# Kernel optimization log

Hardware: AMD Instinct MI355X
Metric: run time of the kernel (lower is better)

## Reference

```python
import jax, jax.numpy as jnp
import numpy as np

B, N, D = 4, 4096, 128
LOSS_WEIGHT = 1.0  # module hardcodes self.loss_weight = 1.0


def setup_inputs() -> dict:
    key = jax.random.key(0)
    k1, k2 = jax.random.split(key)
    corr_pred = jax.random.normal(k1, (B, N, D), dtype=jnp.float32)
    corr_target = jax.random.normal(k2, (B, N, D), dtype=jnp.float32)
    return {"corr_pred": corr_pred, "corr_target": corr_target}


def chamfer_distance(x, y):
    # x: [B, N, D], y: [B, N, D]
    x2 = jnp.sum(x * x, axis=-1)                      # [B, N]  diag of x @ x^T
    y2 = jnp.sum(y * y, axis=-1)                      # [B, N]  diag of y @ y^T
    zz = jnp.einsum('bnd,bmd->bnm', x, y)             # [B, N, N]
    # P[b,i,j] = ||x_i||^2 + ||y_j||^2 - 2 x_i . y_j
    P = x2[:, :, None] + y2[:, None, :] - 2.0 * zz
    P = jnp.clip(P, 0.0, 100.0)
    return jnp.mean(jnp.min(P, axis=1)) + jnp.mean(jnp.min(P, axis=2))


def reference(corr_pred, corr_target):
    chamfer = chamfer_distance(corr_pred, corr_target)
    return LOSS_WEIGHT * chamfer / corr_target.shape[0]
```

## Files before the change

kernel.cpp:

```cpp
#include <hip/hip_runtime.h>
#include <hip/hip_bf16.h>

#define B_ 4
#define N_ 4096
#define D_ 128
#define EPB (N_ * D_)
#define COFF 1024.0f

typedef float f32x4 __attribute__((ext_vector_type(4)));
typedef int   int8v __attribute__((ext_vector_type(8)));
typedef int   int4v __attribute__((ext_vector_type(4)));

#define SQRT2 1.41421356237309515f


__global__ __launch_bounds__(256) void prep_kernel(
    const float* __restrict__ X, const float* __restrict__ Y,
    unsigned char* __restrict__ Xb, unsigned char* __restrict__ Yb,
    float* __restrict__ x2, float* __restrict__ y2,
    int* __restrict__ rowmin, int* __restrict__ colmin)
{
    const int which = blockIdx.y;
    const float* __restrict__ src = which ? Y : X;
    unsigned char* __restrict__ dst = which ? Yb : Xb;
    float* __restrict__ nrm = which ? y2 : x2;
    int* __restrict__ mn = which ? colmin : rowmin;

    const int t = threadIdx.x;
    const int r = t >> 4, c = t & 15;
    const int rgG = blockIdx.x;
    const int row = rgG * 16 + r;

    const float4 v0 = *(const float4*)(src + (size_t)row * D_ + c * 8);
    const float4 v1 = *(const float4*)(src + (size_t)row * D_ + c * 8 + 4);

    float sq = v0.x * v0.x;
    sq = fmaf(v0.y, v0.y, sq); sq = fmaf(v0.z, v0.z, sq); sq = fmaf(v0.w, v0.w, sq);
    sq = fmaf(v1.x, v1.x, sq); sq = fmaf(v1.y, v1.y, sq);
    sq = fmaf(v1.z, v1.z, sq); sq = fmaf(v1.w, v1.w, sq);
    #pragma unroll
    for (int m = 1; m < 16; m <<= 1) sq += __shfl_xor(sq, m);

    unsigned lo = 0, hi = 0;
    lo = __builtin_amdgcn_cvt_pk_fp8_f32(v0.x * SQRT2, v0.y * SQRT2, lo, false);
    lo = __builtin_amdgcn_cvt_pk_fp8_f32(v0.z * SQRT2, v0.w * SQRT2, lo, true);
    hi = __builtin_amdgcn_cvt_pk_fp8_f32(v1.x * SQRT2, v1.y * SQRT2, hi, false);
    hi = __builtin_amdgcn_cvt_pk_fp8_f32(v1.z * SQRT2, v1.w * SQRT2, hi, true);

    const int b = row >> 12;
    const int rg = (row & (N_ - 1)) >> 4;
    uint2 packed; packed.x = lo; packed.y = hi;
    *(uint2*)(dst + (size_t)b * EPB + rg * 2048 + (c >> 2) * 512
              + r * 32 + (c & 3) * 8) = packed;

    if (c == 0) {
        nrm[row] = sq;
        mn[row] = 0x7f7fffff;
    }
}

__global__ __launch_bounds__(256, 2) void chamfer_mfma(
    const unsigned char* __restrict__ Xb, const unsigned char* __restrict__ Yb,
    const float* __restrict__ x2, const float* __restrict__ y2,
    int* __restrict__ rowmin, int* __restrict__ colmin)
{
    const int b = blockIdx.z;
    const int iT = blockIdx.y;
    const int jc = blockIdx.x;
    const int tid = threadIdx.x;
    const int wave = tid >> 6, lane = tid & 63;
    const int quad = lane >> 4, l16 = lane & 15;
    const int rowBase = iT * 256 + wave * 64;

    const unsigned char* __restrict__ Xp = Xb + (size_t)b * EPB;
    const unsigned char* __restrict__ Yp = Yb + (size_t)b * EPB;

    int8v af[4];
    #pragma unroll
    for (int rt = 0; rt < 4; rt++) {
        const unsigned char* ap = Xp + ((rowBase >> 4) + rt) * 2048
                                 + quad * 512 + l16 * 32;
        const int4v lo = *(const int4v*)(ap);
        const int4v hi = *(const int4v*)(ap + 16);
        af[rt] = (int8v){lo.x, lo.y, lo.z, lo.w, hi.x, hi.y, hi.z, hi.w};
    }
    float x2v[4][4];
    #pragma unroll
    for (int rt = 0; rt < 4; rt++)
        #pragma unroll
        for (int i = 0; i < 4; i++)
            x2v[rt][i] = x2[(size_t)b * N_ + rowBase + rt * 16 + quad * 4 + i];

    float rmin[4][4];
    #pragma unroll
    for (int rt = 0; rt < 4; rt++)
        #pragma unroll
        for (int i = 0; i < 4; i++) rmin[rt][i] = 3.0e38f;

    for (int s = 0; s < 4; ++s) {
        const int colBase = jc * 256 + s * 64;
        const int cg = colBase >> 4;

        float y2v[4];
        #pragma unroll
        for (int ct = 0; ct < 4; ct++)
            y2v[ct] = y2[(size_t)b * N_ + colBase + ct * 16 + l16];

        int8v bfv[4];
        #pragma unroll
        for (int ct = 0; ct < 4; ct++) {
            const unsigned char* bp = Yp + (size_t)(cg + ct) * 2048
                                     + quad * 512 + l16 * 32;
            const int4v lo = *(const int4v*)(bp);
            const int4v hi = *(const int4v*)(bp + 16);
            bfv[ct] = (int8v){lo.x, lo.y, lo.z, lo.w, hi.x, hi.y, hi.z, hi.w};
        }

        f32x4 acc[4][4];
        #pragma unroll
        for (int i = 0; i < 4; i++)
            #pragma unroll
            for (int j = 0; j < 4; j++)
                acc[i][j] = (f32x4){0.f, 0.f, 0.f, 0.f};

        #pragma unroll
        for (int rt = 0; rt < 4; rt++)
            #pragma unroll
            for (int ct = 0; ct < 4; ct++)
                acc[rt][ct] = __builtin_amdgcn_mfma_scale_f32_16x16x128_f8f6f4(
                    af[rt], bfv[ct], acc[rt][ct],
                    0, 0,
                    0, 127,
                    0, 127);

        float cmin[4];
        #pragma unroll
        for (int ct = 0; ct < 4; ct++) cmin[ct] = 3.0e38f;
        #pragma unroll
        for (int rt = 0; rt < 4; rt++)
            #pragma unroll
            for (int i = 0; i < 4; i++) {
                const float xv = x2v[rt][i];
                float rm = rmin[rt][i];
                #pragma unroll
                for (int ct = 0; ct < 4; ct++) {
                    const float a = acc[rt][ct][i];
                    rm = fminf(rm, y2v[ct] - a);
                    cmin[ct] = fminf(cmin[ct], xv - a);
                }
                rmin[rt][i] = rm;
            }
        #pragma unroll
        for (int ct = 0; ct < 4; ct++) {
            float v = cmin[ct];
            v = fminf(v, __shfl_xor(v, 16));
            v = fminf(v, __shfl_xor(v, 32));
            if (quad == 0)
                atomicMin(&colmin[(size_t)b * N_ + colBase + ct * 16 + l16],
                          __float_as_int(v + COFF));
        }
    }

    #pragma unroll
    for (int rt = 0; rt < 4; rt++)
        #pragma unroll
        for (int i = 0; i < 4; i++) {
            float v = rmin[rt][i];
            #pragma unroll
            for (int m = 1; m < 16; m <<= 1) v = fminf(v, __shfl_xor(v, m));
            if (l16 == 0) {
                float c = fminf(fmaxf(x2v[rt][i] + v, 0.0f), 100.0f);
                atomicMin(&rowmin[(size_t)b * N_ + rowBase + rt * 16 + quad * 4 + i],
                          __float_as_int(c));
            }
        }
}

__global__ __launch_bounds__(1024) void finalize_kernel(
    const int* __restrict__ rowmin, const int* __restrict__ colmin,
    const float* __restrict__ y2, float* __restrict__ out)
{
    float s = 0.f;
    for (int i = threadIdx.x; i < B_ * N_ / 4; i += 1024) {
        int4 v = ((const int4*)rowmin)[i];
        s += __int_as_float(v.x) + __int_as_float(v.y) +
             __int_as_float(v.z) + __int_as_float(v.w);
        int4 c = ((const int4*)colmin)[i];
        float4 yv = ((const float4*)y2)[i];
        s += fminf(fmaxf(__int_as_float(c.x) - COFF + yv.x, 0.f), 100.f);
        s += fminf(fmaxf(__int_as_float(c.y) - COFF + yv.y, 0.f), 100.f);
        s += fminf(fmaxf(__int_as_float(c.z) - COFF + yv.z, 0.f), 100.f);
        s += fminf(fmaxf(__int_as_float(c.w) - COFF + yv.w, 0.f), 100.f);
    }
    #pragma unroll
    for (int m = 1; m < 64; m <<= 1) s += __shfl_xor(s, m);
    __shared__ float sm[16];
    if ((threadIdx.x & 63) == 0) sm[threadIdx.x >> 6] = s;
    __syncthreads();
    if (threadIdx.x == 0) {
        float t = 0.f;
        #pragma unroll
        for (int i = 0; i < 16; i++) t += sm[i];
        out[0] = t / ((float)B_ * (float)N_) / (float)B_;
    }
}

extern "C" void kernel_launch(void* const* d_in, const int* in_sizes, int n_in,
                              void* d_out, int out_size, void* d_ws, size_t ws_size,
                              hipStream_t stream) {
    const float* X = (const float*)d_in[0];
    const float* Y = (const float*)d_in[1];

    char* ws = (char*)d_ws;
    const size_t f8_bytes = (size_t)B_ * N_ * D_;
    unsigned char* Xb = (unsigned char*)ws;
    unsigned char* Yb = (unsigned char*)(ws + f8_bytes);
    char* ws2 = ws + 2 * f8_bytes;
    const size_t vec_bytes = (size_t)B_ * N_ * 4;
    float* x2     = (float*)(ws2);
    float* y2     = (float*)(ws2 + vec_bytes);
    int*   rowmin = (int*)  (ws2 + 2 * vec_bytes);
    int*   colmin = (int*)  (ws2 + 3 * vec_bytes);
    float* out = (float*)d_out;

    prep_kernel<<<dim3(B_ * N_ / 16, 2), 256, 0, stream>>>(
        X, Y, Xb, Yb, x2, y2, rowmin, colmin);
    chamfer_mfma<<<dim3(16, N_ / 256, B_), 256, 0, stream>>>(
        Xb, Yb, x2, y2, rowmin, colmin);
    finalize_kernel<<<1, 1024, 0, stream>>>(rowmin, colmin, y2, out);
}
```

Before: 92.60 us.

## Prefetch next Y fragment during MFMA and fold y2 into accumulator init

The loads of the next column step's fp8 Y fragments and y2 norms are issued after the current step's MFMAs and before the min-reduction epilogue, with a sched_barrier, so global-load latency overlaps compute. The MFMA accumulators now start at -y2 instead of zero, so the column min already includes the y2 term. This removes one subtract per element in the epilogue and lets finalize skip reading y2. The x2 norms are also loaded as one vector per row tile. The cost is more live registers for the double-buffered fragments, which could pressure occupancy at two blocks per CU.

```diff
diff --git a/kernel.cpp b/kernel.cpp
--- a/kernel.cpp
+++ b/kernel.cpp
@@ -84,12 +84,10 @@
         const int4v hi = *(const int4v*)(ap + 16);
         af[rt] = (int8v){lo.x, lo.y, lo.z, lo.w, hi.x, hi.y, hi.z, hi.w};
     }
-    float x2v[4][4];
+    f32x4 x2v[4];
     #pragma unroll
     for (int rt = 0; rt < 4; rt++)
-        #pragma unroll
-        for (int i = 0; i < 4; i++)
-            x2v[rt][i] = x2[(size_t)b * N_ + rowBase + rt * 16 + quad * 4 + i];
+        x2v[rt] = *(const f32x4*)(x2 + (size_t)b * N_ + rowBase + rt * 16 + quad * 4);
 
     float rmin[4][4];
     #pragma unroll
@@ -97,16 +95,10 @@
         #pragma unroll
         for (int i = 0; i < 4; i++) rmin[rt][i] = 3.0e38f;
 
-    for (int s = 0; s < 4; ++s) {
-        const int colBase = jc * 256 + s * 64;
-        const int cg = colBase >> 4;
-
-        float y2v[4];
-        #pragma unroll
-        for (int ct = 0; ct < 4; ct++)
-            y2v[ct] = y2[(size_t)b * N_ + colBase + ct * 16 + l16];
-
-        int8v bfv[4];
+    int8v bfv[4];
+    float y2v[4];
+    {
+        const int cg = (jc * 256) >> 4;
         #pragma unroll
         for (int ct = 0; ct < 4; ct++) {
             const unsigned char* bp = Yp + (size_t)(cg + ct) * 2048
@@ -114,14 +106,21 @@
             const int4v lo = *(const int4v*)(bp);
             const int4v hi = *(const int4v*)(bp + 16);
             bfv[ct] = (int8v){lo.x, lo.y, lo.z, lo.w, hi.x, hi.y, hi.z, hi.w};
-        }
+            y2v[ct] = y2[(size_t)b * N_ + jc * 256 + ct * 16 + l16];
+        }
+    }
+
+    for (int s = 0; s < 4; ++s) {
+        const int colBase = jc * 256 + s * 64;
 
         f32x4 acc[4][4];
         #pragma unroll
-        for (int i = 0; i < 4; i++)
-            #pragma unroll
-            for (int j = 0; j < 4; j++)
-                acc[i][j] = (f32x4){0.f, 0.f, 0.f, 0.f};
+        for (int ct = 0; ct < 4; ct++) {
+            const float ny = -y2v[ct];
+            #pragma unroll
+            for (int rt = 0; rt < 4; rt++)
+                acc[rt][ct] = (f32x4){ny, ny, ny, ny};
+        }
 
         #pragma unroll
         for (int rt = 0; rt < 4; rt++)
@@ -133,6 +132,20 @@
                     0, 127,
                     0, 127);
 
+        if (s < 3) {
+            const int cg = (colBase + 64) >> 4;
+            #pragma unroll
+            for (int ct = 0; ct < 4; ct++) {
+                const unsigned char* bp = Yp + (size_t)(cg + ct) * 2048
+                                         + quad * 512 + l16 * 32;
+                const int4v lo = *(const int4v*)(bp);
+                const int4v hi = *(const int4v*)(bp + 16);
+                bfv[ct] = (int8v){lo.x, lo.y, lo.z, lo.w, hi.x, hi.y, hi.z, hi.w};
+                y2v[ct] = y2[(size_t)b * N_ + colBase + 64 + ct * 16 + l16];
+            }
+        }
+        __builtin_amdgcn_sched_barrier(0);
+
         float cmin[4];
         #pragma unroll
         for (int ct = 0; ct < 4; ct++) cmin[ct] = 3.0e38f;
@@ -145,7 +158,7 @@
                 #pragma unroll
                 for (int ct = 0; ct < 4; ct++) {
                     const float a = acc[rt][ct][i];
-                    rm = fminf(rm, y2v[ct] - a);
+                    rm = fminf(rm, -a);
                     cmin[ct] = fminf(cmin[ct], xv - a);
                 }
                 rmin[rt][i] = rm;
@@ -178,7 +191,7 @@
 
 __global__ __launch_bounds__(1024) void finalize_kernel(
     const int* __restrict__ rowmin, const int* __restrict__ colmin,
-    const float* __restrict__ y2, float* __restrict__ out)
+    float* __restrict__ out)
 {
     float s = 0.f;
     for (int i = threadIdx.x; i < B_ * N_ / 4; i += 1024) {
@@ -186,11 +199,10 @@
         s += __int_as_float(v.x) + __int_as_float(v.y) +
              __int_as_float(v.z) + __int_as_float(v.w);
         int4 c = ((const int4*)colmin)[i];
-        float4 yv = ((const float4*)y2)[i];
-        s += fminf(fmaxf(__int_as_float(c.x) - COFF + yv.x, 0.f), 100.f);
-        s += fminf(fmaxf(__int_as_float(c.y) - COFF + yv.y, 0.f), 100.f);
-        s += fminf(fmaxf(__int_as_float(c.z) - COFF + yv.z, 0.f), 100.f);
-        s += fminf(fmaxf(__int_as_float(c.w) - COFF + yv.w, 0.f), 100.f);
+        s += fminf(fmaxf(__int_as_float(c.x) - COFF, 0.f), 100.f);
+        s += fminf(fmaxf(__int_as_float(c.y) - COFF, 0.f), 100.f);
+        s += fminf(fmaxf(__int_as_float(c.z) - COFF, 0.f), 100.f);
+        s += fminf(fmaxf(__int_as_float(c.w) - COFF, 0.f), 100.f);
     }
     #pragma unroll
     for (int m = 1; m < 64; m <<= 1) s += __shfl_xor(s, m);
@@ -227,5 +239,5 @@
         X, Y, Xb, Yb, x2, y2, rowmin, colmin);
     chamfer_mfma<<<dim3(16, N_ / 256, B_), 256, 0, stream>>>(
         Xb, Yb, x2, y2, rowmin, colmin);
-    finalize_kernel<<<1, 1024, 0, stream>>>(rowmin, colmin, y2, out);
-}
+    finalize_kernel<<<1, 1024, 0, stream>>>(rowmin, colmin, out);
+}
```

New measurement: 132.1 us. +42.6%, slower.

## Split MFMA accumulation into column halves and parallelize final reduction

Applied to the files above, without the earlier changes.

The 4x4 accumulator tile per 64-column step is processed as two 4x2 halves, so each half's MFMA results are reduced to row/column minima before the next half is computed. This lowers peak accumulator register pressure and may let min reduction interleave with MFMA work. The single-block finalize is also split into a 16-block partial-sum kernel plus a tiny second kernel. That adds one extra launch in exchange for more parallel reads of the min arrays.

```diff
diff --git a/kernel.cpp b/kernel.cpp
--- a/kernel.cpp
+++ b/kernel.cpp
@@ -8,6 +8,7 @@
 #define COFF 1024.0f
 
 typedef float f32x4 __attribute__((ext_vector_type(4)));
+typedef float f32x2 __attribute__((ext_vector_type(2)));
 typedef int   int8v __attribute__((ext_vector_type(8)));
 typedef int   int4v __attribute__((ext_vector_type(4)));
 
@@ -116,48 +117,52 @@
             bfv[ct] = (int8v){lo.x, lo.y, lo.z, lo.w, hi.x, hi.y, hi.z, hi.w};
         }
 
-        f32x4 acc[4][4];
-        #pragma unroll
-        for (int i = 0; i < 4; i++)
-            #pragma unroll
-            for (int j = 0; j < 4; j++)
-                acc[i][j] = (f32x4){0.f, 0.f, 0.f, 0.f};
-
-        #pragma unroll
-        for (int rt = 0; rt < 4; rt++)
-            #pragma unroll
-            for (int ct = 0; ct < 4; ct++)
-                acc[rt][ct] = __builtin_amdgcn_mfma_scale_f32_16x16x128_f8f6f4(
-                    af[rt], bfv[ct], acc[rt][ct],
-                    0, 0,
-                    0, 127,
-                    0, 127);
-
-        float cmin[4];
-        #pragma unroll
-        for (int ct = 0; ct < 4; ct++) cmin[ct] = 3.0e38f;
-        #pragma unroll
-        for (int rt = 0; rt < 4; rt++)
-            #pragma unroll
-            for (int i = 0; i < 4; i++) {
-                const float xv = x2v[rt][i];
-                float rm = rmin[rt][i];
+        #pragma unroll
+        for (int h = 0; h < 2; ++h) {
+            f32x4 acc[4][2];
+            #pragma unroll
+            for (int i = 0; i < 4; i++)
                 #pragma unroll
-                for (int ct = 0; ct < 4; ct++) {
-                    const float a = acc[rt][ct][i];
-                    rm = fminf(rm, y2v[ct] - a);
-                    cmin[ct] = fminf(cmin[ct], xv - a);
+                for (int j = 0; j < 2; j++)
+                    acc[i][j] = (f32x4){0.f, 0.f, 0.f, 0.f};
+
+            #pragma unroll
+            for (int rt = 0; rt < 4; rt++)
+                #pragma unroll
+                for (int c2 = 0; c2 < 2; c2++)
+                    acc[rt][c2] = __builtin_amdgcn_mfma_scale_f32_16x16x128_f8f6f4(
+                        af[rt], bfv[h * 2 + c2], acc[rt][c2],
+                        0, 0,
+                        0, 127,
+                        0, 127);
+
+            float cmin[2];
+            #pragma unroll
+            for (int c2 = 0; c2 < 2; c2++) cmin[c2] = 3.0e38f;
+            #pragma unroll
+            for (int rt = 0; rt < 4; rt++)
+                #pragma unroll
+                for (int i = 0; i < 4; i++) {
+                    const float xv = x2v[rt][i];
+                    float rm = rmin[rt][i];
+                    #pragma unroll
+                    for (int c2 = 0; c2 < 2; c2++) {
+                        const float a = acc[rt][c2][i];
+                        rm = fminf(rm, y2v[h * 2 + c2] - a);
+                        cmin[c2] = fminf(cmin[c2], xv - a);
+                    }
+                    rmin[rt][i] = rm;
                 }
-                rmin[rt][i] = rm;
+            #pragma unroll
+            for (int c2 = 0; c2 < 2; c2++) {
+                float v = cmin[c2];
+                v = fminf(v, __shfl_xor(v, 16));
+                v = fminf(v, __shfl_xor(v, 32));
+                if (quad == 0)
+                    atomicMin(&colmin[(size_t)b * N_ + colBase
+                                      + (h * 2 + c2) * 16 + l16],
+                              __float_as_int(v + COFF));
             }
-        #pragma unroll
-        for (int ct = 0; ct < 4; ct++) {
-            float v = cmin[ct];
-            v = fminf(v, __shfl_xor(v, 16));
-            v = fminf(v, __shfl_xor(v, 32));
-            if (quad == 0)
-                atomicMin(&colmin[(size_t)b * N_ + colBase + ct * 16 + l16],
-                          __float_as_int(v + COFF));
         }
     }
 
@@ -176,14 +181,15 @@
         }
 }
 
-__global__ __launch_bounds__(1024) void finalize_kernel(
+__global__ __launch_bounds__(256) void finalize1_kernel(
     const int* __restrict__ rowmin, const int* __restrict__ colmin,
-    const float* __restrict__ y2, float* __restrict__ out)
-{
-    float s = 0.f;
-    for (int i = threadIdx.x; i < B_ * N_ / 4; i += 1024) {
+    const float* __restrict__ y2, float* __restrict__ partial)
+{
+    const int i = blockIdx.x * 256 + threadIdx.x;
+    float s;
+    {
         int4 v = ((const int4*)rowmin)[i];
-        s += __int_as_float(v.x) + __int_as_float(v.y) +
+        s  = __int_as_float(v.x) + __int_as_float(v.y) +
              __int_as_float(v.z) + __int_as_float(v.w);
         int4 c = ((const int4*)colmin)[i];
         float4 yv = ((const float4*)y2)[i];
@@ -194,15 +200,22 @@
     }
     #pragma unroll
     for (int m = 1; m < 64; m <<= 1) s += __shfl_xor(s, m);
-    __shared__ float sm[16];
+    __shared__ float sm[4];
     if ((threadIdx.x & 63) == 0) sm[threadIdx.x >> 6] = s;
     __syncthreads();
-    if (threadIdx.x == 0) {
-        float t = 0.f;
-        #pragma unroll
-        for (int i = 0; i < 16; i++) t += sm[i];
-        out[0] = t / ((float)B_ * (float)N_) / (float)B_;
-    }
+    if (threadIdx.x == 0)
+        partial[blockIdx.x] = sm[0] + sm[1] + sm[2] + sm[3];
+}
+
+__global__ __launch_bounds__(64) void finalize2_kernel(
+    const float* __restrict__ partial, float* __restrict__ out)
+{
+    const int l = threadIdx.x;
+    float s = (l < 16) ? partial[l] : 0.f;
+    #pragma unroll
+    for (int m = 1; m < 16; m <<= 1) s += __shfl_xor(s, m);
+    if (l == 0)
+        out[0] = s / ((float)B_ * (float)N_) / (float)B_;
 }
 
 extern "C" void kernel_launch(void* const* d_in, const int* in_sizes, int n_in,
@@ -217,15 +230,17 @@
     unsigned char* Yb = (unsigned char*)(ws + f8_bytes);
     char* ws2 = ws + 2 * f8_bytes;
     const size_t vec_bytes = (size_t)B_ * N_ * 4;
-    float* x2     = (float*)(ws2);
-    float* y2     = (float*)(ws2 + vec_bytes);
-    int*   rowmin = (int*)  (ws2 + 2 * vec_bytes);
-    int*   colmin = (int*)  (ws2 + 3 * vec_bytes);
+    float* x2      = (float*)(ws2);
+    float* y2      = (float*)(ws2 + vec_bytes);
+    int*   rowmin  = (int*)  (ws2 + 2 * vec_bytes);
+    int*   colmin  = (int*)  (ws2 + 3 * vec_bytes);
+    float* partial = (float*)(ws2 + 4 * vec_bytes);
     float* out = (float*)d_out;
 
     prep_kernel<<<dim3(B_ * N_ / 16, 2), 256, 0, stream>>>(
         X, Y, Xb, Yb, x2, y2, rowmin, colmin);
     chamfer_mfma<<<dim3(16, N_ / 256, B_), 256, 0, stream>>>(
         Xb, Yb, x2, y2, rowmin, colmin);
-    finalize_kernel<<<1, 1024, 0, stream>>>(rowmin, colmin, y2, out);
-}
+    finalize1_kernel<<<16, 256, 0, stream>>>(rowmin, colmin, y2, partial);
+    finalize2_kernel<<<1, 64, 0, stream>>>(partial, out);
+}
```

Result: no change. 90.92 us (-1.8%).
